# Performance work log

Hardware: AMD Instinct MI355X
Metric: run time of the kernel (lower is better)

## Reference

```python
import jax, jax.numpy as jnp
import numpy as np

TOP_K = 2  # MoE top-k routing


def setup_inputs() -> dict:
    key = jax.random.key(0)
    ks = jax.random.split(key, 5)
    B, D, H, O, N = 8192, 3072, 128, 10, 8
    scale_g = 1.0 / np.sqrt(D)
    return {
        "x": jax.random.normal(ks[0], (B, D), dtype=jnp.float32),
        "Wg": jax.random.normal(ks[1], (D, N), dtype=jnp.float32) * scale_g,
        "bg": jnp.zeros((N,), dtype=jnp.float32),
        "W1": jax.random.normal(ks[2], (N, D, H), dtype=jnp.float32) * scale_g,
        "b1": jnp.zeros((N, H), dtype=jnp.float32),
        "W2": jax.random.normal(ks[3], (N, H, O), dtype=jnp.float32) * (1.0 / np.sqrt(H)),
        "b2": jnp.zeros((N, O), dtype=jnp.float32),
    }


def reference(x, Wg, bg, W1, b1, W2, b2):
    # Gating: logits -> top-k -> softmax over the k selected logits
    g = x @ Wg + bg                                  # [B, N]
    tv, ti = jax.lax.top_k(g, TOP_K)                 # [B, k]
    w = jax.nn.softmax(tv, axis=-1)                  # [B, k]
    # Expert MLPs, computed densely over all experts (vectorized dispatch)
    h = jax.nn.relu(jnp.einsum('bd,edh->beh', x, W1) + b1)   # [B, N, H]
    y = jnp.einsum('beh,eho->beo', h, W2) + b2               # [B, N, O]
    # Combine: gather each token's k selected expert outputs, weight, sum
    ysel = jnp.take_along_axis(y, ti[:, :, None], axis=1)    # [B, k, O]
    return jnp.sum(w[:, :, None] * ysel, axis=1)             # [B, O]
```

## Files before the change

### kernel.cpp

```cpp
#include <hip/hip_runtime.h>
#include <hip/hip_bf16.h>

#define B_TOK 8192
#define D_DIM 3072
#define H_DIM 128
#define O_DIM 10
#define N_EXP 8

#define BM 128
#define BK 64
#define HLDS_STRIDE 136

typedef __bf16 bf16x8 __attribute__((ext_vector_type(8)));
typedef float  f32x4  __attribute__((ext_vector_type(4)));

__device__ __forceinline__ unsigned short f2bf(float f) {
  unsigned int u = __float_as_uint(f);
  unsigned int r = (u + 0x7FFFu + ((u >> 16) & 1u)) >> 16;
  return (unsigned short)r;
}

__device__ __forceinline__ void async16(const void* g, void* l) {
  __builtin_amdgcn_global_load_lds(
      (const __attribute__((address_space(1))) void*)g,
      (__attribute__((address_space(3))) void*)l,
      16, 0, 0);
}

__global__ void k0_w1_transpose(const float* __restrict__ W1,
                                unsigned short* __restrict__ w1t) {
  __shared__ unsigned short tile[32][33];
  const int e  = blockIdx.z;
  const int d0 = blockIdx.x * 32;
  const int h0 = blockIdx.y * 32;
  const int tx = threadIdx.x;
  const int ty = threadIdx.y;
  const float* src = W1 + ((size_t)e * D_DIM + d0) * H_DIM + h0;
#pragma unroll
  for (int k = 0; k < 4; ++k) {
    int r = ty + 8 * k;
    tile[r][tx] = f2bf(src[(size_t)r * H_DIM + tx]);
  }
  __syncthreads();
  unsigned short* dst = w1t + ((size_t)e * H_DIM + h0) * D_DIM + d0;
#pragma unroll
  for (int k = 0; k < 4; ++k) {
    int r = ty + 8 * k;
    dst[(size_t)r * D_DIM + tx] = tile[tx][r];
  }
}

__global__ __launch_bounds__(512) void k1_gate_convert(
    const float* __restrict__ x, const float* __restrict__ Wg,
    const float* __restrict__ bg, unsigned short* __restrict__ xb,
    int4* __restrict__ idx4, float2* __restrict__ wts, int* __restrict__ cnt) {
  __shared__ float wg_lds[N_EXP * D_DIM];
  __shared__ int lcnt[N_EXP], gbase[N_EXP];
  const int tid = threadIdx.x;

  if (tid < N_EXP) lcnt[tid] = 0;
  for (int f = tid; f < D_DIM * N_EXP / 4; f += 512) {
    const float4 v = ((const float4*)Wg)[f];
    const int d  = f >> 1;
    const int nh = (f & 1) * 4;
    wg_lds[(nh + 0) * D_DIM + d] = v.x;
    wg_lds[(nh + 1) * D_DIM + d] = v.y;
    wg_lds[(nh + 2) * D_DIM + d] = v.z;
    wg_lds[(nh + 3) * D_DIM + d] = v.w;
  }
  __syncthreads();

  const int lane = tid & 63;
  const int wv   = tid >> 6;
  const int tk0  = blockIdx.x * 32 + wv * 4;

  const float* xr0 = x + (size_t)(tk0 + 0) * D_DIM;
  const float* xr1 = x + (size_t)(tk0 + 1) * D_DIM;
  const float* xr2 = x + (size_t)(tk0 + 2) * D_DIM;
  const float* xr3 = x + (size_t)(tk0 + 3) * D_DIM;
  unsigned short* xw0 = xb + (size_t)(tk0 + 0) * D_DIM;
  unsigned short* xw1 = xb + (size_t)(tk0 + 1) * D_DIM;
  unsigned short* xw2 = xb + (size_t)(tk0 + 2) * D_DIM;
  unsigned short* xw3 = xb + (size_t)(tk0 + 3) * D_DIM;

  float acc[4][N_EXP];
#pragma unroll
  for (int t = 0; t < 4; ++t)
#pragma unroll
    for (int n = 0; n < N_EXP; ++n) acc[t][n] = 0.f;

#pragma unroll 2
  for (int jj = 0; jj < D_DIM / 64; ++jj) {
    const int d = jj * 64 + lane;
    float w8[N_EXP];
#pragma unroll
    for (int n = 0; n < N_EXP; ++n) w8[n] = wg_lds[n * D_DIM + d];
    const float x0 = xr0[d], x1 = xr1[d], x2 = xr2[d], x3 = xr3[d];
    xw0[d] = f2bf(x0); xw1[d] = f2bf(x1); xw2[d] = f2bf(x2); xw3[d] = f2bf(x3);
#pragma unroll
    for (int n = 0; n < N_EXP; ++n) {
      acc[0][n] = fmaf(x0, w8[n], acc[0][n]);
      acc[1][n] = fmaf(x1, w8[n], acc[1][n]);
      acc[2][n] = fmaf(x2, w8[n], acc[2][n]);
      acc[3][n] = fmaf(x3, w8[n], acc[3][n]);
    }
  }

#pragma unroll
  for (int t = 0; t < 4; ++t)
#pragma unroll
    for (int n = 0; n < N_EXP; ++n) {
#pragma unroll
      for (int off = 32; off > 0; off >>= 1)
        acc[t][n] += __shfl_xor(acc[t][n], off, 64);
    }

  int li0[4], li1[4], lp0[4], lp1[4];
  float lw0[4], lw1[4];
  if (lane == 0) {
#pragma unroll
    for (int t = 0; t < 4; ++t) {
      float g[N_EXP];
#pragma unroll
      for (int n = 0; n < N_EXP; ++n) g[n] = acc[t][n] + bg[n];
      int i0 = 0;
#pragma unroll
      for (int n = 1; n < N_EXP; ++n) if (g[n] > g[i0]) i0 = n;
      int i1 = (i0 == 0) ? 1 : 0;
#pragma unroll
      for (int n = 0; n < N_EXP; ++n) if (n != i0 && g[n] > g[i1]) i1 = n;
      float e1 = expf(g[i1] - g[i0]);
      float inv = 1.f / (1.f + e1);
      li0[t] = i0; li1[t] = i1;
      lw0[t] = inv; lw1[t] = e1 * inv;
      lp0[t] = atomicAdd(&lcnt[i0], 1);
      lp1[t] = atomicAdd(&lcnt[i1], 1);
    }
  }
  __syncthreads();
  if (tid < N_EXP) gbase[tid] = atomicAdd(&cnt[tid], lcnt[tid]);
  __syncthreads();
  if (lane == 0) {
#pragma unroll
    for (int t = 0; t < 4; ++t) {
      idx4[tk0 + t] = make_int4(li0[t], gbase[li0[t]] + lp0[t],
                                li1[t], gbase[li1[t]] + lp1[t]);
      wts[tk0 + t]  = make_float2(lw0[t], lw1[t]);
    }
  }
}

__global__ __launch_bounds__(256) void k1b_scan_scatter(
    const int* __restrict__ cnt, int* __restrict__ off_g,
    const int4* __restrict__ idx4, int* __restrict__ tlist) {
  __shared__ int off[N_EXP + 1];
  if (threadIdx.x == 0) {
    int s = 0;
#pragma unroll
    for (int n = 0; n < N_EXP; ++n) { off[n] = s; s += cnt[n]; }
    off[N_EXP] = s;
#pragma unroll
    for (int n = 0; n <= N_EXP; ++n) off_g[n] = off[n];
  }
  __syncthreads();
  for (int t = threadIdx.x; t < B_TOK; t += 256) {
    const int4 r = idx4[t];
    tlist[off[r.x] + r.y] = t;
    tlist[off[r.z] + r.w] = t;
  }
}

__global__ __launch_bounds__(256) void k2_experts(
    const unsigned short* __restrict__ xb,
    const unsigned short* __restrict__ w1t,
    const float* __restrict__ b1,
    const float* __restrict__ W2,
    const float* __restrict__ b2,
    const int* __restrict__ cnt, const int* __restrict__ off_g,
    const int* __restrict__ tlist,
    float* __restrict__ ypair) {
  const int e    = blockIdx.y;
  const int n_e  = cnt[e];
  const int row0 = blockIdx.x * BM;
  if (row0 >= n_e) return;
  const int off_e = off_g[e];

  __shared__ __align__(16) unsigned short sm[(34816 + 4096) / 2];
  unsigned short* a_lds   = sm;
  unsigned short* b_lds   = sm + 128 * 64;
  unsigned short* h_lds   = sm;
  unsigned short* w2t_lds = sm + 128 * HLDS_STRIDE;

  const int tid  = threadIdx.x;
  const int lane = tid & 63;
  const int wv   = tid >> 6;

  const float* W2e = W2 + (size_t)e * H_DIM * O_DIM;
  for (int idx = tid; idx < 16 * 128; idx += 256) {
    int o = idx >> 7, hh = idx & 127;
    float v = (o < O_DIM) ? W2e[hh * O_DIM + o] : 0.f;
    w2t_lds[idx] = f2bf(v);
  }

  const int mhalf = (wv >> 1) * 64;
  const int nhalf = (wv & 1) * 64;

  f32x4 acc[4][4];
#pragma unroll
  for (int i = 0; i < 4; ++i)
#pragma unroll
    for (int j = 0; j < 4; ++j)
      acc[i][j] = (f32x4){0.f, 0.f, 0.f, 0.f};

  const int srow = wv * 32 + (lane >> 3);
  const int scol = (lane & 7) * 8;

  const unsigned short* Arow[4];
#pragma unroll
  for (int j = 0; j < 4; ++j) {
    int gr = row0 + srow + j * 8;
    gr = gr < n_e ? gr : n_e - 1;
    Arow[j] = xb + (size_t)tlist[off_e + gr] * D_DIM + scol;
  }
  const unsigned short* Bt_base = w1t + (size_t)e * H_DIM * D_DIM + scol;

  for (int k0 = 0; k0 < D_DIM; k0 += BK) {
#pragma unroll
    for (int j = 0; j < 4; ++j) {
      const int r = srow + j * 8;
      async16(Arow[j] + k0, a_lds + (wv * 32 + j * 8) * BK);
      async16(Bt_base + (size_t)r * D_DIM + k0, b_lds + (wv * 32 + j * 8) * BK);
    }
    __syncthreads();
#pragma unroll
    for (int kk = 0; kk < 2; ++kk) {
      bf16x8 af[4], bfr[4];
      const int krd = kk * 32 + (lane >> 4) * 8;
#pragma unroll
      for (int mi = 0; mi < 4; ++mi)
        af[mi] = *(const bf16x8*)(a_lds + (mhalf + mi * 16 + (lane & 15)) * BK + krd);
#pragma unroll
      for (int ni = 0; ni < 4; ++ni)
        bfr[ni] = *(const bf16x8*)(b_lds + (nhalf + ni * 16 + (lane & 15)) * BK + krd);
#pragma unroll
      for (int mi = 0; mi < 4; ++mi)
#pragma unroll
        for (int ni = 0; ni < 4; ++ni)
          acc[mi][ni] = __builtin_amdgcn_mfma_f32_16x16x32_bf16(af[mi], bfr[ni], acc[mi][ni], 0, 0, 0);
    }
    __syncthreads();
  }

  const float* b1e = b1 + e * H_DIM;
#pragma unroll
  for (int ni = 0; ni < 4; ++ni) {
    const int col  = nhalf + ni * 16 + (lane & 15);
    const float bias = b1e[col];
#pragma unroll
    for (int mi = 0; mi < 4; ++mi) {
      const int rbase = mhalf + mi * 16 + ((lane >> 4) << 2);
#pragma unroll
      for (int r = 0; r < 4; ++r) {
        float v = acc[mi][ni][r] + bias;
        v = v > 0.f ? v : 0.f;
        h_lds[(rbase + r) * HLDS_STRIDE + col] = f2bf(v);
      }
    }
  }
  __syncthreads();

  f32x4 acc2[2];
  acc2[0] = (f32x4){0.f, 0.f, 0.f, 0.f};
  acc2[1] = (f32x4){0.f, 0.f, 0.f, 0.f};
#pragma unroll
  for (int ks = 0; ks < 4; ++ks) {
    const int krd = ks * 32 + (lane >> 4) * 8;
    bf16x8 bfr = *(const bf16x8*)(w2t_lds + (lane & 15) * 128 + krd);
#pragma unroll
    for (int mi = 0; mi < 2; ++mi) {
      bf16x8 afr = *(const bf16x8*)(h_lds + (wv * 32 + mi * 16 + (lane & 15)) * HLDS_STRIDE + krd);
      acc2[mi] = __builtin_amdgcn_mfma_f32_16x16x32_bf16(afr, bfr, acc2[mi], 0, 0, 0);
    }
  }
  const int o = lane & 15;
  if (o < O_DIM) {
    const float bias2 = b2[e * O_DIM + o];
#pragma unroll
    for (int mi = 0; mi < 2; ++mi) {
#pragma unroll
      for (int r = 0; r < 4; ++r) {
        const int rl = wv * 32 + mi * 16 + ((lane >> 4) << 2) + r;
        if (row0 + rl < n_e)
          ypair[(size_t)(off_e + row0 + rl) * 16 + o] = acc2[mi][r] + bias2;
      }
    }
  }
}

__global__ __launch_bounds__(256) void k3_combine(
    const float* __restrict__ ypair, const int4* __restrict__ idx4,
    const float2* __restrict__ wts, const int* __restrict__ off_g,
    float* __restrict__ out) {
  const int g = blockIdx.x * 256 + threadIdx.x;
  if (g >= B_TOK * O_DIM) return;
  const int b = g / O_DIM, o = g - b * O_DIM;
  const int4 r = idx4[b];
  const float2 w = wts[b];
  out[g] = w.x * ypair[(size_t)(off_g[r.x] + r.y) * 16 + o] +
           w.y * ypair[(size_t)(off_g[r.z] + r.w) * 16 + o];
}

extern "C" void kernel_launch(void* const* d_in, const int* in_sizes, int n_in,
                              void* d_out, int out_size, void* d_ws, size_t ws_size,
                              hipStream_t stream) {
  const float* x  = (const float*)d_in[0];
  const float* Wg = (const float*)d_in[1];
  const float* bg = (const float*)d_in[2];
  const float* W1 = (const float*)d_in[3];
  const float* b1 = (const float*)d_in[4];
  const float* W2 = (const float*)d_in[5];
  const float* b2 = (const float*)d_in[6];
  float* out = (float*)d_out;

  char* ws = (char*)d_ws;
  unsigned short* xb  = (unsigned short*)ws;
  unsigned short* w1t = (unsigned short*)(ws + 50331648);
  int4*   idx4  = (int4*)  (ws + 56623104);
  float2* wts   = (float2*)(ws + 56754176);
  int*    cnt   = (int*)   (ws + 56819712);
  int*    off_g = (int*)   (ws + 56819744);
  int*    tlist = (int*)   (ws + 56819840);
  float*  ypair = (float*) (ws + 56885376);

  k0_w1_transpose<<<dim3(96, 4, 8), dim3(32, 8), 0, stream>>>(W1, w1t);
  hipMemsetAsync(cnt, 0, N_EXP * sizeof(int), stream);
  k1_gate_convert<<<dim3(B_TOK / 32), dim3(512), 0, stream>>>(x, Wg, bg, xb, idx4, wts, cnt);
  k1b_scan_scatter<<<dim3(1), dim3(256), 0, stream>>>(cnt, off_g, idx4, tlist);
  k2_experts<<<dim3(B_TOK / BM, N_EXP), dim3(256), 0, stream>>>(
      xb, w1t, b1, W2, b2, cnt, off_g, tlist, ypair);
  k3_combine<<<dim3((B_TOK * O_DIM + 255) / 256), dim3(256), 0, stream>>>(
      ypair, idx4, wts, off_g, out);
}
```

Measured before the change: 283.5 us.

## Double-buffer expert GEMM with BK=128, vectorize W1 transpose, parallelize scatter

The expert GEMM now uses a double-buffered LDS pipeline with K-tile 128, issuing async loads for the next stage before computing the current one. This removes the second barrier per iteration and is meant to hide global load latency. The W1 transpose uses 64x64 tiles with 16-byte vector stores. The single-block scan/scatter is split into a tiny scan kernel (with BM-padded offsets) and a grid-wide scatter. The larger LDS footprint limits occupancy to roughly one block per CU.

```diff
diff --git a/kernel.cpp b/kernel.cpp
--- a/kernel.cpp
+++ b/kernel.cpp
@@ -8,11 +8,12 @@
 #define N_EXP 8
 
 #define BM 128
-#define BK 64
+#define BK2 128
 #define HLDS_STRIDE 136
 
 typedef __bf16 bf16x8 __attribute__((ext_vector_type(8)));
 typedef float  f32x4  __attribute__((ext_vector_type(4)));
+typedef unsigned short us8 __attribute__((ext_vector_type(8)));
 
 __device__ __forceinline__ unsigned short f2bf(float f) {
   unsigned int u = __float_as_uint(f);
@@ -27,26 +28,33 @@
       16, 0, 0);
 }
 
-__global__ void k0_w1_transpose(const float* __restrict__ W1,
-                                unsigned short* __restrict__ w1t) {
-  __shared__ unsigned short tile[32][33];
+__global__ __launch_bounds__(256) void k0_w1_transpose(const float* __restrict__ W1,
+                                                       unsigned short* __restrict__ w1t) {
+  __shared__ __align__(16) unsigned short lds[64 * 72];
   const int e  = blockIdx.z;
-  const int d0 = blockIdx.x * 32;
-  const int h0 = blockIdx.y * 32;
-  const int tx = threadIdx.x;
-  const int ty = threadIdx.y;
+  const int d0 = blockIdx.x * 64;
+  const int h0 = blockIdx.y * 64;
+  const int tid = threadIdx.x;
+
   const float* src = W1 + ((size_t)e * D_DIM + d0) * H_DIM + h0;
-#pragma unroll
-  for (int k = 0; k < 4; ++k) {
-    int r = ty + 8 * k;
-    tile[r][tx] = f2bf(src[(size_t)r * H_DIM + tx]);
-  }
-  __syncthreads();
+  const int hl = tid & 63;
+  const int dg = tid >> 6;
+#pragma unroll
+  for (int k = 0; k < 16; ++k) {
+    const int d = dg + 4 * k;
+    lds[hl * 72 + d] = f2bf(src[(size_t)d * H_DIM + hl]);
+  }
+  __syncthreads();
+
   unsigned short* dst = w1t + ((size_t)e * H_DIM + h0) * D_DIM + d0;
-#pragma unroll
-  for (int k = 0; k < 4; ++k) {
-    int r = ty + 8 * k;
-    dst[(size_t)r * D_DIM + tx] = tile[tx][r];
+  const int q  = tid & 7;
+  const int h1 = tid >> 3;
+#pragma unroll
+  for (int k = 0; k < 2; ++k) {
+    const int h = h1 + 32 * k;
+    const int d = q * 8;
+    us8 v = *(const us8*)(lds + h * 72 + d);
+    *(us8*)(dst + (size_t)h * D_DIM + d) = v;
   }
 }
 
@@ -150,24 +158,26 @@
   }
 }
 
-__global__ __launch_bounds__(256) void k1b_scan_scatter(
-    const int* __restrict__ cnt, int* __restrict__ off_g,
-    const int4* __restrict__ idx4, int* __restrict__ tlist) {
-  __shared__ int off[N_EXP + 1];
+__global__ void k1b1_scan(const int* __restrict__ cnt, int* __restrict__ off_g) {
   if (threadIdx.x == 0) {
     int s = 0;
 #pragma unroll
-    for (int n = 0; n < N_EXP; ++n) { off[n] = s; s += cnt[n]; }
-    off[N_EXP] = s;
-#pragma unroll
-    for (int n = 0; n <= N_EXP; ++n) off_g[n] = off[n];
-  }
-  __syncthreads();
-  for (int t = threadIdx.x; t < B_TOK; t += 256) {
-    const int4 r = idx4[t];
-    tlist[off[r.x] + r.y] = t;
-    tlist[off[r.z] + r.w] = t;
-  }
+    for (int n = 0; n < N_EXP; ++n) {
+      off_g[n] = s;
+      s += (cnt[n] + BM - 1) / BM * BM;
+    }
+    off_g[N_EXP] = s;
+  }
+}
+
+__global__ __launch_bounds__(256) void k1b2_scatter(
+    const int* __restrict__ off_g, const int4* __restrict__ idx4,
+    int* __restrict__ tlist) {
+  const int t = blockIdx.x * 256 + threadIdx.x;
+  if (t >= B_TOK) return;
+  const int4 r = idx4[t];
+  tlist[off_g[r.x] + r.y] = t;
+  tlist[off_g[r.z] + r.w] = t;
 }
 
 __global__ __launch_bounds__(256) void k2_experts(
@@ -185,11 +195,9 @@
   if (row0 >= n_e) return;
   const int off_e = off_g[e];
 
-  __shared__ __align__(16) unsigned short sm[(34816 + 4096) / 2];
-  unsigned short* a_lds   = sm;
-  unsigned short* b_lds   = sm + 128 * 64;
+  __shared__ __align__(16) unsigned short sm[65536 + 2048];
   unsigned short* h_lds   = sm;
-  unsigned short* w2t_lds = sm + 128 * HLDS_STRIDE;
+  unsigned short* w2t_lds = sm + 65536;
 
   const int tid  = threadIdx.x;
   const int lane = tid & 63;
@@ -212,44 +220,58 @@
     for (int j = 0; j < 4; ++j)
       acc[i][j] = (f32x4){0.f, 0.f, 0.f, 0.f};
 
-  const int srow = wv * 32 + (lane >> 3);
-  const int scol = (lane & 7) * 8;
-
-  const unsigned short* Arow[4];
-#pragma unroll
-  for (int j = 0; j < 4; ++j) {
-    int gr = row0 + srow + j * 8;
+  const int quad = lane >> 4;
+  const int koff0 = (lane & 15) * 8;
+  const unsigned short* Abase[8];
+  const unsigned short* Bbase[8];
+#pragma unroll
+  for (int j = 0; j < 8; ++j) {
+    int rloc = wv * 32 + j * 4 + quad;
+    int gr = row0 + rloc;
     gr = gr < n_e ? gr : n_e - 1;
-    Arow[j] = xb + (size_t)tlist[off_e + gr] * D_DIM + scol;
-  }
-  const unsigned short* Bt_base = w1t + (size_t)e * H_DIM * D_DIM + scol;
-
-  for (int k0 = 0; k0 < D_DIM; k0 += BK) {
-#pragma unroll
-    for (int j = 0; j < 4; ++j) {
-      const int r = srow + j * 8;
-      async16(Arow[j] + k0, a_lds + (wv * 32 + j * 8) * BK);
-      async16(Bt_base + (size_t)r * D_DIM + k0, b_lds + (wv * 32 + j * 8) * BK);
-    }
+    Abase[j] = xb + (size_t)tlist[off_e + gr] * D_DIM + koff0;
+    Bbase[j] = w1t + ((size_t)e * H_DIM + rloc) * D_DIM + koff0;
+  }
+
+#define STAGE(it, pp)                                                     \
+  {                                                                       \
+    const int ko = (it) * BK2;                                            \
+    unsigned short* abuf = sm + (pp) * 32768;                             \
+    unsigned short* bbuf = sm + 16384 + (pp) * 32768;                     \
+    _Pragma("unroll")                                                     \
+    for (int j = 0; j < 8; ++j) {                                         \
+      const int ldsrow = (wv * 32 + j * 4) * BK2;                         \
+      async16(Abase[j] + ko, abuf + ldsrow);                              \
+      async16(Bbase[j] + ko, bbuf + ldsrow);                              \
+    }                                                                     \
+  }
+
+  STAGE(0, 0);
+
+  const int NIT = D_DIM / BK2;
+  for (int it = 0; it < NIT; ++it) {
     __syncthreads();
-#pragma unroll
-    for (int kk = 0; kk < 2; ++kk) {
+    if (it + 1 < NIT) STAGE(it + 1, (it + 1) & 1);
+    const unsigned short* al = sm + (it & 1) * 32768;
+    const unsigned short* bl = sm + 16384 + (it & 1) * 32768;
+#pragma unroll
+    for (int kk = 0; kk < 4; ++kk) {
+      const int krd = kk * 32 + quad * 8;
       bf16x8 af[4], bfr[4];
-      const int krd = kk * 32 + (lane >> 4) * 8;
 #pragma unroll
       for (int mi = 0; mi < 4; ++mi)
-        af[mi] = *(const bf16x8*)(a_lds + (mhalf + mi * 16 + (lane & 15)) * BK + krd);
+        af[mi] = *(const bf16x8*)(al + (mhalf + mi * 16 + (lane & 15)) * BK2 + krd);
 #pragma unroll
       for (int ni = 0; ni < 4; ++ni)
-        bfr[ni] = *(const bf16x8*)(b_lds + (nhalf + ni * 16 + (lane & 15)) * BK + krd);
+        bfr[ni] = *(const bf16x8*)(bl + (nhalf + ni * 16 + (lane & 15)) * BK2 + krd);
 #pragma unroll
       for (int mi = 0; mi < 4; ++mi)
 #pragma unroll
         for (int ni = 0; ni < 4; ++ni)
           acc[mi][ni] = __builtin_amdgcn_mfma_f32_16x16x32_bf16(af[mi], bfr[ni], acc[mi][ni], 0, 0, 0);
     }
-    __syncthreads();
-  }
+  }
+  __syncthreads();
 
   const float* b1e = b1 + e * H_DIM;
 #pragma unroll
@@ -258,7 +280,7 @@
     const float bias = b1e[col];
 #pragma unroll
     for (int mi = 0; mi < 4; ++mi) {
-      const int rbase = mhalf + mi * 16 + ((lane >> 4) << 2);
+      const int rbase = mhalf + mi * 16 + (quad << 2);
 #pragma unroll
       for (int r = 0; r < 4; ++r) {
         float v = acc[mi][ni][r] + bias;
@@ -274,7 +296,7 @@
   acc2[1] = (f32x4){0.f, 0.f, 0.f, 0.f};
 #pragma unroll
   for (int ks = 0; ks < 4; ++ks) {
-    const int krd = ks * 32 + (lane >> 4) * 8;
+    const int krd = ks * 32 + quad * 8;
     bf16x8 bfr = *(const bf16x8*)(w2t_lds + (lane & 15) * 128 + krd);
 #pragma unroll
     for (int mi = 0; mi < 2; ++mi) {
@@ -289,7 +311,7 @@
     for (int mi = 0; mi < 2; ++mi) {
 #pragma unroll
       for (int r = 0; r < 4; ++r) {
-        const int rl = wv * 32 + mi * 16 + ((lane >> 4) << 2) + r;
+        const int rl = wv * 32 + mi * 16 + (quad << 2) + r;
         if (row0 + rl < n_e)
           ypair[(size_t)(off_e + row0 + rl) * 16 + o] = acc2[mi][r] + bias2;
       }
@@ -328,14 +350,15 @@
   int4*   idx4  = (int4*)  (ws + 56623104);
   float2* wts   = (float2*)(ws + 56754176);
   int*    cnt   = (int*)   (ws + 56819712);
-  int*    off_g = (int*)   (ws + 56819744);
-  int*    tlist = (int*)   (ws + 56819840);
-  float*  ypair = (float*) (ws + 56885376);
-
-  k0_w1_transpose<<<dim3(96, 4, 8), dim3(32, 8), 0, stream>>>(W1, w1t);
-  hipMemsetAsync(cnt, 0, N_EXP * sizeof(int), stream);
+  int*    off_g = (int*)   (ws + 56819840);
+  int*    tlist = (int*)   (ws + 56819968);
+  float*  ypair = (float*) (ws + 56890112);
+
+  k0_w1_transpose<<<dim3(48, 2, 8), dim3(256), 0, stream>>>(W1, w1t);
+  (void)hipMemsetAsync(cnt, 0, N_EXP * sizeof(int), stream);
   k1_gate_convert<<<dim3(B_TOK / 32), dim3(512), 0, stream>>>(x, Wg, bg, xb, idx4, wts, cnt);
-  k1b_scan_scatter<<<dim3(1), dim3(256), 0, stream>>>(cnt, off_g, idx4, tlist);
+  k1b1_scan<<<dim3(1), dim3(64), 0, stream>>>(cnt, off_g);
+  k1b2_scatter<<<dim3(B_TOK / 256), dim3(256), 0, stream>>>(off_g, idx4, tlist);
   k2_experts<<<dim3(B_TOK / BM, N_EXP), dim3(256), 0, stream>>>(
       xb, w1t, b1, W2, b2, cnt, off_g, tlist, ypair);
   k3_combine<<<dim3((B_TOK * O_DIM + 255) / 256), dim3(256), 0, stream>>>(
```

After: 270.6 us. -4.5%, faster.
